# Optimization experiments

Measured on AMD Instinct MI355X. Metric: run time of the kernel, lower is better.

## Reference

```python
import jax, jax.numpy as jnp
import numpy as np

D = 3072      # hidden_dim == flattened CIFAR image size
KF = 1        # FourierFeature k (default, KAN_FourierAttention does not pass k)
NP = 5        # module-level n -> size of w and n parameter vectors
NC = 100      # num_classes
B = 512


def setup_inputs() -> dict:
    key = jax.random.key(0)
    ks = jax.random.split(key, 7)
    return {
        "x": jax.random.normal(ks[0], (B, 3, 32, 32), dtype=jnp.float32),
        "a": jax.random.normal(ks[1], (D, D, KF), dtype=jnp.float32),
        "b": jax.random.normal(ks[2], (D, D, KF), dtype=jnp.float32),
        "w": jax.random.normal(ks[3], (NP,), dtype=jnp.float32),
        "n_param": jax.random.normal(ks[4], (NP,), dtype=jnp.float32),
        "fc_w": jax.random.normal(ks[5], (NC, D), dtype=jnp.float32) * 0.02,
        "fc_b": jax.random.normal(ks[6], (NC,), dtype=jnp.float32) * 0.02,
    }


def reference(x, a, b, w, n_param, fc_w, fc_b):
    xf = x.reshape(x.shape[0], -1)                 # [B, D]
    m = jnp.arange(1, KF + 1, dtype=xf.dtype)      # [KF]
    cos_part = jnp.cos(xf[..., None] * m)          # [B, D, KF]
    sin_part = jnp.sin(xf[..., None] * m)          # [B, D, KF]
    # Original: result[b,i,j] = sum_k cos[b,j,k]*a[i,j,k] + sin[b,j,k]*b[i,j,k]
    # then part2[b,j] = sum_i result[b,i,j].  Fuse both reductions (over i and k)
    # to avoid materializing the [B, D, D, KF] broadcast intermediate.
    part2 = (jnp.einsum('bdk,idk->bd', cos_part, a)
             + jnp.einsum('bdk,idk->bd', sin_part, b))   # [B, D]
    # part1: scalar accumulated over i=1..len(n)-1
    part1 = jnp.sum(w[1:] * n_param[1:] + w[:-1] * n_param[:-1])
    Z = part1 + part2                               # [B, D]
    return Z @ fc_w.T + fc_b                        # [B, NC]
```

## Files before the change

kernel.cpp:

```cpp
#include <hip/hip_runtime.h>
#include <math.h>

#define D 3072
#define BATCH 512
#define NCLS 100
#define NPAD 112
#define KS 16
#define KCHUNK (D / KS)

typedef __attribute__((ext_vector_type(8))) short bf16x8;
typedef __attribute__((ext_vector_type(4))) float f32x4;

#define WS_OFF_W   24576
#define WS_OFF_Z   712704
#define WS_OFF_P   3858432
#define WS_NEED    (WS_OFF_P + (size_t)KS * BATCH * NPAD * 4)

__device__ inline unsigned short f2bf(float f) {
    unsigned u = __float_as_uint(f);
    u += 0x7FFF + ((u >> 16) & 1);
    return (unsigned short)(u >> 16);
}

__global__ __launch_bounds__(256) void colsum_kernel(const float* __restrict__ a,
                                                     const float* __restrict__ b,
                                                     float* __restrict__ ws) {
    const int col  = blockIdx.y * 1024 + threadIdx.x * 4;
    const int row0 = blockIdx.x * 32;

    float4 sa = make_float4(0.f, 0.f, 0.f, 0.f);
    float4 sb = make_float4(0.f, 0.f, 0.f, 0.f);
    #pragma unroll
    for (int r = 0; r < 32; ++r) {
        const int i = row0 + r;
        const float4 va = *(const float4*)(a + i * D + col);
        const float4 vb = *(const float4*)(b + i * D + col);
        sa.x += va.x; sa.y += va.y; sa.z += va.z; sa.w += va.w;
        sb.x += vb.x; sb.y += vb.y; sb.z += vb.z; sb.w += vb.w;
    }
    atomicAdd(&ws[col + 0], sa.x);
    atomicAdd(&ws[col + 1], sa.y);
    atomicAdd(&ws[col + 2], sa.z);
    atomicAdd(&ws[col + 3], sa.w);
    atomicAdd(&ws[D + col + 0], sb.x);
    atomicAdd(&ws[D + col + 1], sb.y);
    atomicAdd(&ws[D + col + 2], sb.z);
    atomicAdd(&ws[D + col + 3], sb.w);
}

__global__ __launch_bounds__(256) void convw_kernel(const float* __restrict__ fcw,
                                                    unsigned short* __restrict__ Wb) {
    const int idx = blockIdx.x * 256 + threadIdx.x;
    const int c  = idx / (D / 4);
    const int d  = (idx % (D / 4)) * 4;
    ushort4 o;
    if (c < NCLS) {
        const float4 v = *(const float4*)(fcw + c * D + d);
        o.x = f2bf(v.x); o.y = f2bf(v.y); o.z = f2bf(v.z); o.w = f2bf(v.w);
    } else {
        o.x = o.y = o.z = o.w = 0;
    }
    *(ushort4*)(Wb + c * D + d) = o;
}

__global__ __launch_bounds__(256) void zgen_kernel(const float* __restrict__ x,
                                                   const float* __restrict__ w5,
                                                   const float* __restrict__ n5,
                                                   const float* __restrict__ ws,
                                                   unsigned short* __restrict__ Zb) {
    const int idx = blockIdx.x * 256 + threadIdx.x;
    const int b = idx / (D / 4);
    const int d = (idx % (D / 4)) * 4;

    float part1 = 0.f;
    #pragma unroll
    for (int i = 0; i < 4; ++i)
        part1 += w5[i + 1] * n5[i + 1] + w5[i] * n5[i];

    const float4 xv = *(const float4*)(x + b * D + d);
    const float4 Av = *(const float4*)(ws + d);
    const float4 Bv = *(const float4*)(ws + D + d);

    float sv, cv;
    ushort4 o;
    __sincosf(xv.x, &sv, &cv); o.x = f2bf(part1 + cv * Av.x + sv * Bv.x);
    __sincosf(xv.y, &sv, &cv); o.y = f2bf(part1 + cv * Av.y + sv * Bv.y);
    __sincosf(xv.z, &sv, &cv); o.z = f2bf(part1 + cv * Av.z + sv * Bv.z);
    __sincosf(xv.w, &sv, &cv); o.w = f2bf(part1 + cv * Av.w + sv * Bv.w);
    *(ushort4*)(Zb + b * D + d) = o;
}

__global__ __launch_bounds__(256) void mfma_gemm_kernel(
        const unsigned short* __restrict__ Zb,
        const unsigned short* __restrict__ Wb,
        float* __restrict__ part) {
    const int wave = threadIdx.x >> 6;
    const int lane = threadIdx.x & 63;
    const int l16  = lane & 15;
    const int quad = lane >> 4;
    const int m0   = blockIdx.x * 64 + wave * 16;
    const int kbase = blockIdx.y * KCHUNK + quad * 8;

    f32x4 acc[7];
    #pragma unroll
    for (int n = 0; n < 7; ++n) acc[n] = (f32x4){0.f, 0.f, 0.f, 0.f};

    const unsigned short* za = Zb + (m0 + l16) * D + kbase;
    const unsigned short* wb = Wb + l16 * D + kbase;

    #pragma unroll
    for (int kk = 0; kk < KCHUNK; kk += 32) {
        const bf16x8 af = *(const bf16x8*)(za + kk);
        #pragma unroll
        for (int n = 0; n < 7; ++n) {
            const bf16x8 bf = *(const bf16x8*)(wb + n * 16 * D + kk);
            acc[n] = __builtin_amdgcn_mfma_f32_16x16x32_bf16(af, bf, acc[n], 0, 0, 0);
        }
    }

    float* pb = part + (size_t)blockIdx.y * (BATCH * NPAD);
    #pragma unroll
    for (int n = 0; n < 7; ++n)
        #pragma unroll
        for (int r = 0; r < 4; ++r)
            pb[(m0 + quad * 4 + r) * NPAD + n * 16 + l16] = acc[n][r];
}

__global__ __launch_bounds__(256) void reduce2_kernel(const float* __restrict__ part,
                                                      const float* __restrict__ fcb,
                                                      float* __restrict__ out) {
    const int idx = blockIdx.x * 256 + threadIdx.x;
    if (idx >= BATCH * NCLS) return;
    const int b = idx / NCLS;
    const int c = idx % NCLS;
    float s = fcb[c];
    #pragma unroll
    for (int ks = 0; ks < KS; ++ks)
        s += part[ks * (BATCH * NPAD) + b * NPAD + c];
    out[idx] = s;
}

__global__ __launch_bounds__(256) void fused_gemm_kernel(
        const float* __restrict__ x,
        const float* __restrict__ w5,
        const float* __restrict__ n5,
        const float* __restrict__ fcw,
        const float* __restrict__ fcb,
        const float* __restrict__ ws,
        float* __restrict__ out) {
    __shared__ __align__(16) float Zl[32 * 36];
    __shared__ __align__(16) float Wl[32 * 132];

    const int t  = threadIdx.x;
    const int bt = blockIdx.x;
    const int j  = blockIdx.y;
    const float* __restrict__ A = ws;
    const float* __restrict__ B = ws + D;

    float part1 = 0.f;
    #pragma unroll
    for (int i = 0; i < 4; ++i)
        part1 += w5[i + 1] * n5[i + 1] + w5[i] * n5[i];

    const int c0 = (t & 31) * 4;
    const int b0 = (t >> 5) * 4;
    const int kl = t & 31;
    const int tg = t >> 5;
    const int bbase = bt * 32;

    float acc[4][4];
    #pragma unroll
    for (int i = 0; i < 4; ++i)
        #pragma unroll
        for (int q = 0; q < 4; ++q) acc[i][q] = 0.f;

    for (int s = 0; s < 3; ++s) {
        const int dbase = j * 96 + s * 32;
        for (int idx = t; idx < NCLS * 32; idx += 256) {
            const int c = idx >> 5;
            const int k = idx & 31;
            Wl[k * 132 + c] = fcw[c * D + dbase + k];
        }
        const float Av = A[dbase + kl];
        const float Bv = B[dbase + kl];
        #pragma unroll
        for (int i = 0; i < 4; ++i) {
            const int bl = tg + i * 8;
            const float xv = x[(bbase + bl) * D + dbase + kl];
            float sv, cv;
            sincosf(xv, &sv, &cv);
            Zl[bl * 36 + kl] = part1 + cv * Av + sv * Bv;
        }
        __syncthreads();
        #pragma unroll
        for (int k = 0; k < 32; ++k) {
            const float4 wv = *(const float4*)&Wl[k * 132 + c0];
            float zb[4];
            #pragma unroll
            for (int bj = 0; bj < 4; ++bj) zb[bj] = Zl[(b0 + bj) * 36 + k];
            #pragma unroll
            for (int bj = 0; bj < 4; ++bj) {
                acc[bj][0] += zb[bj] * wv.x;
                acc[bj][1] += zb[bj] * wv.y;
                acc[bj][2] += zb[bj] * wv.z;
                acc[bj][3] += zb[bj] * wv.w;
            }
        }
        __syncthreads();
    }

    if (c0 < NCLS) {
        #pragma unroll
        for (int bj = 0; bj < 4; ++bj) {
            const int row = bbase + b0 + bj;
            #pragma unroll
            for (int q = 0; q < 4; ++q) {
                const int c = c0 + q;
                if (c < NCLS) {
                    float v = acc[bj][q];
                    if (j == 0) v += fcb[c];
                    atomicAdd(&out[row * NCLS + c], v);
                }
            }
        }
    }
}

extern "C" void kernel_launch(void* const* d_in, const int* in_sizes, int n_in,
                              void* d_out, int out_size, void* d_ws, size_t ws_size,
                              hipStream_t stream) {
    const float* x   = (const float*)d_in[0];
    const float* a   = (const float*)d_in[1];
    const float* b   = (const float*)d_in[2];
    const float* w5  = (const float*)d_in[3];
    const float* n5  = (const float*)d_in[4];
    const float* fcw = (const float*)d_in[5];
    const float* fcb = (const float*)d_in[6];
    float* out = (float*)d_out;
    float* wsf = (float*)d_ws;

    hipMemsetAsync(d_ws, 0, 2 * D * sizeof(float), stream);
    colsum_kernel<<<dim3(96, 3), 256, 0, stream>>>(a, b, wsf);

    if (ws_size >= WS_NEED) {
        unsigned short* Wb = (unsigned short*)((char*)d_ws + WS_OFF_W);
        unsigned short* Zb = (unsigned short*)((char*)d_ws + WS_OFF_Z);
        float*          Pp = (float*)((char*)d_ws + WS_OFF_P);
        convw_kernel<<<dim3(336), 256, 0, stream>>>(fcw, Wb);
        zgen_kernel<<<dim3(1536), 256, 0, stream>>>(x, w5, n5, wsf, Zb);
        mfma_gemm_kernel<<<dim3(8, KS), 256, 0, stream>>>(Zb, Wb, Pp);
        reduce2_kernel<<<dim3(200), 256, 0, stream>>>(Pp, fcb, out);
    } else {
        hipMemsetAsync(d_out, 0, (size_t)out_size * sizeof(float), stream);
        fused_gemm_kernel<<<dim3(16, 32), 256, 0, stream>>>(x, w5, n5, fcw, fcb,
                                                            wsf, out);
    }
}
```

Baseline: 133.4 us.

## Fuse Z generation into MFMA GEMM and merge colsum with weight conversion

Measured after the change: 127.7 us. -4.3%, faster.

```diff
diff --git a/kernel.cpp b/kernel.cpp
--- a/kernel.cpp
+++ b/kernel.cpp
@@ -5,15 +5,14 @@
 #define BATCH 512
 #define NCLS 100
 #define NPAD 112
-#define KS 16
+#define KS 32
 #define KCHUNK (D / KS)
 
 typedef __attribute__((ext_vector_type(8))) short bf16x8;
 typedef __attribute__((ext_vector_type(4))) float f32x4;
 
 #define WS_OFF_W   24576
-#define WS_OFF_Z   712704
-#define WS_OFF_P   3858432
+#define WS_OFF_P   712704
 #define WS_NEED    (WS_OFF_P + (size_t)KS * BATCH * NPAD * 4)
 
 __device__ inline unsigned short f2bf(float f) {
@@ -22,76 +21,56 @@
     return (unsigned short)(u >> 16);
 }
 
-__global__ __launch_bounds__(256) void colsum_kernel(const float* __restrict__ a,
-                                                     const float* __restrict__ b,
-                                                     float* __restrict__ ws) {
-    const int col  = blockIdx.y * 1024 + threadIdx.x * 4;
-    const int row0 = blockIdx.x * 32;
-
-    float4 sa = make_float4(0.f, 0.f, 0.f, 0.f);
-    float4 sb = make_float4(0.f, 0.f, 0.f, 0.f);
-    #pragma unroll
-    for (int r = 0; r < 32; ++r) {
-        const int i = row0 + r;
-        const float4 va = *(const float4*)(a + i * D + col);
-        const float4 vb = *(const float4*)(b + i * D + col);
-        sa.x += va.x; sa.y += va.y; sa.z += va.z; sa.w += va.w;
-        sb.x += vb.x; sb.y += vb.y; sb.z += vb.z; sb.w += vb.w;
-    }
-    atomicAdd(&ws[col + 0], sa.x);
-    atomicAdd(&ws[col + 1], sa.y);
-    atomicAdd(&ws[col + 2], sa.z);
-    atomicAdd(&ws[col + 3], sa.w);
-    atomicAdd(&ws[D + col + 0], sb.x);
-    atomicAdd(&ws[D + col + 1], sb.y);
-    atomicAdd(&ws[D + col + 2], sb.z);
-    atomicAdd(&ws[D + col + 3], sb.w);
-}
-
-__global__ __launch_bounds__(256) void convw_kernel(const float* __restrict__ fcw,
-                                                    unsigned short* __restrict__ Wb) {
-    const int idx = blockIdx.x * 256 + threadIdx.x;
-    const int c  = idx / (D / 4);
-    const int d  = (idx % (D / 4)) * 4;
-    ushort4 o;
-    if (c < NCLS) {
-        const float4 v = *(const float4*)(fcw + c * D + d);
-        o.x = f2bf(v.x); o.y = f2bf(v.y); o.z = f2bf(v.z); o.w = f2bf(v.w);
+__global__ __launch_bounds__(256) void prep_kernel(const float* __restrict__ a,
+                                                   const float* __restrict__ b,
+                                                   const float* __restrict__ fcw,
+                                                   float* __restrict__ ws,
+                                                   unsigned short* __restrict__ Wb) {
+    const int bid = blockIdx.x;
+    const int t   = threadIdx.x;
+    if (bid < 288) {
+        const int rc   = bid / 3;
+        const int cg   = bid % 3;
+        const int col  = cg * 1024 + t * 4;
+        const int row0 = rc * 32;
+        float4 sa = make_float4(0.f, 0.f, 0.f, 0.f);
+        float4 sb = make_float4(0.f, 0.f, 0.f, 0.f);
+        #pragma unroll
+        for (int r = 0; r < 32; ++r) {
+            const int i = row0 + r;
+            const float4 va = *(const float4*)(a + i * D + col);
+            const float4 vb = *(const float4*)(b + i * D + col);
+            sa.x += va.x; sa.y += va.y; sa.z += va.z; sa.w += va.w;
+            sb.x += vb.x; sb.y += vb.y; sb.z += vb.z; sb.w += vb.w;
+        }
+        atomicAdd(&ws[col + 0], sa.x);
+        atomicAdd(&ws[col + 1], sa.y);
+        atomicAdd(&ws[col + 2], sa.z);
+        atomicAdd(&ws[col + 3], sa.w);
+        atomicAdd(&ws[D + col + 0], sb.x);
+        atomicAdd(&ws[D + col + 1], sb.y);
+        atomicAdd(&ws[D + col + 2], sb.z);
+        atomicAdd(&ws[D + col + 3], sb.w);
     } else {
-        o.x = o.y = o.z = o.w = 0;
-    }
-    *(ushort4*)(Wb + c * D + d) = o;
-}
-
-__global__ __launch_bounds__(256) void zgen_kernel(const float* __restrict__ x,
-                                                   const float* __restrict__ w5,
-                                                   const float* __restrict__ n5,
-                                                   const float* __restrict__ ws,
-                                                   unsigned short* __restrict__ Zb) {
-    const int idx = blockIdx.x * 256 + threadIdx.x;
-    const int b = idx / (D / 4);
-    const int d = (idx % (D / 4)) * 4;
-
-    float part1 = 0.f;
-    #pragma unroll
-    for (int i = 0; i < 4; ++i)
-        part1 += w5[i + 1] * n5[i + 1] + w5[i] * n5[i];
-
-    const float4 xv = *(const float4*)(x + b * D + d);
-    const float4 Av = *(const float4*)(ws + d);
-    const float4 Bv = *(const float4*)(ws + D + d);
-
-    float sv, cv;
-    ushort4 o;
-    __sincosf(xv.x, &sv, &cv); o.x = f2bf(part1 + cv * Av.x + sv * Bv.x);
-    __sincosf(xv.y, &sv, &cv); o.y = f2bf(part1 + cv * Av.y + sv * Bv.y);
-    __sincosf(xv.z, &sv, &cv); o.z = f2bf(part1 + cv * Av.z + sv * Bv.z);
-    __sincosf(xv.w, &sv, &cv); o.w = f2bf(part1 + cv * Av.w + sv * Bv.w);
-    *(ushort4*)(Zb + b * D + d) = o;
-}
-
-__global__ __launch_bounds__(256) void mfma_gemm_kernel(
-        const unsigned short* __restrict__ Zb,
+        const int idx = (bid - 288) * 256 + t;
+        const int c   = idx / (D / 4);
+        const int d   = (idx % (D / 4)) * 4;
+        ushort4 o;
+        if (c < NCLS) {
+            const float4 v = *(const float4*)(fcw + c * D + d);
+            o.x = f2bf(v.x); o.y = f2bf(v.y); o.z = f2bf(v.z); o.w = f2bf(v.w);
+        } else {
+            o.x = o.y = o.z = o.w = 0;
+        }
+        *(ushort4*)(Wb + c * D + d) = o;
+    }
+}
+
+__global__ __launch_bounds__(256) void fzgemm_kernel(
+        const float* __restrict__ x,
+        const float* __restrict__ w5,
+        const float* __restrict__ n5,
+        const float* __restrict__ ws,
         const unsigned short* __restrict__ Wb,
         float* __restrict__ part) {
     const int wave = threadIdx.x >> 6;
@@ -99,26 +78,49 @@
     const int l16  = lane & 15;
     const int quad = lane >> 4;
     const int m0   = blockIdx.x * 64 + wave * 16;
-    const int kbase = blockIdx.y * KCHUNK + quad * 8;
+    const int j    = blockIdx.y;
+    const int kb   = j * KCHUNK + quad * 8;
+
+    float part1 = 0.f;
+    #pragma unroll
+    for (int i = 0; i < 4; ++i)
+        part1 += w5[i + 1] * n5[i + 1] + w5[i] * n5[i];
 
     f32x4 acc[7];
     #pragma unroll
     for (int n = 0; n < 7; ++n) acc[n] = (f32x4){0.f, 0.f, 0.f, 0.f};
 
-    const unsigned short* za = Zb + (m0 + l16) * D + kbase;
-    const unsigned short* wb = Wb + l16 * D + kbase;
+    const float* xr = x + (m0 + l16) * D;
 
     #pragma unroll
     for (int kk = 0; kk < KCHUNK; kk += 32) {
-        const bf16x8 af = *(const bf16x8*)(za + kk);
+        const int col = kb + kk;
+        const float4 xv0 = *(const float4*)(xr + col);
+        const float4 xv1 = *(const float4*)(xr + col + 4);
+        const float4 Av0 = *(const float4*)(ws + col);
+        const float4 Av1 = *(const float4*)(ws + col + 4);
+        const float4 Bv0 = *(const float4*)(ws + D + col);
+        const float4 Bv1 = *(const float4*)(ws + D + col + 4);
+
+        union { bf16x8 v; unsigned short s[8]; } af;
+        float sv, cv;
+        __sincosf(xv0.x, &sv, &cv); af.s[0] = f2bf(part1 + cv * Av0.x + sv * Bv0.x);
+        __sincosf(xv0.y, &sv, &cv); af.s[1] = f2bf(part1 + cv * Av0.y + sv * Bv0.y);
+        __sincosf(xv0.z, &sv, &cv); af.s[2] = f2bf(part1 + cv * Av0.z + sv * Bv0.z);
+        __sincosf(xv0.w, &sv, &cv); af.s[3] = f2bf(part1 + cv * Av0.w + sv * Bv0.w);
+        __sincosf(xv1.x, &sv, &cv); af.s[4] = f2bf(part1 + cv * Av1.x + sv * Bv1.x);
+        __sincosf(xv1.y, &sv, &cv); af.s[5] = f2bf(part1 + cv * Av1.y + sv * Bv1.y);
+        __sincosf(xv1.z, &sv, &cv); af.s[6] = f2bf(part1 + cv * Av1.z + sv * Bv1.z);
+        __sincosf(xv1.w, &sv, &cv); af.s[7] = f2bf(part1 + cv * Av1.w + sv * Bv1.w);
+
         #pragma unroll
         for (int n = 0; n < 7; ++n) {
-            const bf16x8 bf = *(const bf16x8*)(wb + n * 16 * D + kk);
-            acc[n] = __builtin_amdgcn_mfma_f32_16x16x32_bf16(af, bf, acc[n], 0, 0, 0);
-        }
-    }
-
-    float* pb = part + (size_t)blockIdx.y * (BATCH * NPAD);
+            const bf16x8 bf = *(const bf16x8*)(Wb + (n * 16 + l16) * D + col);
+            acc[n] = __builtin_amdgcn_mfma_f32_16x16x32_bf16(af.v, bf, acc[n], 0, 0, 0);
+        }
+    }
+
+    float* pb = part + (size_t)j * (BATCH * NPAD);
     #pragma unroll
     for (int n = 0; n < 7; ++n)
         #pragma unroll
@@ -150,30 +152,23 @@
         float* __restrict__ out) {
     __shared__ __align__(16) float Zl[32 * 36];
     __shared__ __align__(16) float Wl[32 * 132];
-
     const int t  = threadIdx.x;
     const int bt = blockIdx.x;
     const int j  = blockIdx.y;
-    const float* __restrict__ A = ws;
-    const float* __restrict__ B = ws + D;
-
     float part1 = 0.f;
     #pragma unroll
     for (int i = 0; i < 4; ++i)
         part1 += w5[i + 1] * n5[i + 1] + w5[i] * n5[i];
-
     const int c0 = (t & 31) * 4;
     const int b0 = (t >> 5) * 4;
     const int kl = t & 31;
     const int tg = t >> 5;
     const int bbase = bt * 32;
-
     float acc[4][4];
     #pragma unroll
     for (int i = 0; i < 4; ++i)
         #pragma unroll
         for (int q = 0; q < 4; ++q) acc[i][q] = 0.f;
-
     for (int s = 0; s < 3; ++s) {
         const int dbase = j * 96 + s * 32;
         for (int idx = t; idx < NCLS * 32; idx += 256) {
@@ -181,8 +176,8 @@
             const int k = idx & 31;
             Wl[k * 132 + c] = fcw[c * D + dbase + k];
         }
-        const float Av = A[dbase + kl];
-        const float Bv = B[dbase + kl];
+        const float Av = ws[dbase + kl];
+        const float Bv = ws[D + dbase + kl];
         #pragma unroll
         for (int i = 0; i < 4; ++i) {
             const int bl = tg + i * 8;
@@ -208,7 +203,6 @@
         }
         __syncthreads();
     }
-
     if (c0 < NCLS) {
         #pragma unroll
         for (int bj = 0; bj < 4; ++bj) {
@@ -240,18 +234,17 @@
     float* wsf = (float*)d_ws;
 
     hipMemsetAsync(d_ws, 0, 2 * D * sizeof(float), stream);
-    colsum_kernel<<<dim3(96, 3), 256, 0, stream>>>(a, b, wsf);
 
     if (ws_size >= WS_NEED) {
         unsigned short* Wb = (unsigned short*)((char*)d_ws + WS_OFF_W);
-        unsigned short* Zb = (unsigned short*)((char*)d_ws + WS_OFF_Z);
         float*          Pp = (float*)((char*)d_ws + WS_OFF_P);
-        convw_kernel<<<dim3(336), 256, 0, stream>>>(fcw, Wb);
-        zgen_kernel<<<dim3(1536), 256, 0, stream>>>(x, w5, n5, wsf, Zb);
-        mfma_gemm_kernel<<<dim3(8, KS), 256, 0, stream>>>(Zb, Wb, Pp);
+        prep_kernel<<<dim3(624), 256, 0, stream>>>(a, b, fcw, wsf, Wb);
+        fzgemm_kernel<<<dim3(8, KS), 256, 0, stream>>>(x, w5, n5, wsf, Wb, Pp);
         reduce2_kernel<<<dim3(200), 256, 0, stream>>>(Pp, fcb, out);
     } else {
         hipMemsetAsync(d_out, 0, (size_t)out_size * sizeof(float), stream);
+        prep_kernel<<<dim3(288), 256, 0, stream>>>(a, b, fcw, wsf,
+                                                   (unsigned short*)out );
         fused_gemm_kernel<<<dim3(16, 32), 256, 0, stream>>>(x, w5, n5, fcw, fcb,
                                                             wsf, out);
     }
```
